# Kernel optimization log

Hardware: AMD Instinct MI355X
Metric: run time of the kernel (lower is better)

The kernel has to match this reference:

```python
import jax, jax.numpy as jnp
import numpy as np

VOCAB = 50000
DIM = 300
BATCH = 1024
CTX = 10


def setup_inputs() -> dict:
    key = jax.random.key(0)
    k1, k2, k3, k4 = jax.random.split(key, 4)
    context = jax.random.randint(k1, (BATCH, CTX), 0, VOCAB, dtype=jnp.int64 if jax.config.read('jax_enable_x64') else jnp.int32)
    W_proj = jax.random.normal(k2, (DIM, VOCAB), dtype=jnp.float32) * 0.02
    W_cls = jax.random.normal(k3, (VOCAB, DIM), dtype=jnp.float32) * 0.02
    b_cls = jax.random.normal(k4, (VOCAB,), dtype=jnp.float32) * 0.02
    return {"context": context, "W_proj": W_proj, "W_cls": W_cls, "b_cls": b_cls, "pad_idx": 0}


def reference(context, W_proj, W_cls, b_cls, pad_idx):
    # One-hot @ W_proj.T == gather of W_proj columns at context ids: [B, C, D]
    emb = jnp.take(W_proj, context, axis=1)            # [D, B, C]
    emb = jnp.moveaxis(emb, 0, -1)                     # [B, C, D]
    # zeroing the pad_idx column of the one-hot kills pad tokens' contribution,
    # but the mean still divides by the full context length C.
    mask = (context != pad_idx).astype(emb.dtype)      # [B, C]
    emb = emb * mask[..., None]
    pooled = emb.mean(axis=1)                          # [B, D]
    logits = pooled @ W_cls.T + b_cls                  # [B, V]
    return jax.nn.log_softmax(logits, axis=1)
```

## Files before the change

kernel.cpp:

```cpp
#include <hip/hip_runtime.h>
#include <math.h>

#define B_SZ 1024
#define CTXL 10
#define DIM  300
#define VOC  50000
#define KP   320
#define NTIL 391
#define NSG  50
#define WROW 1200
#define WMAXOFF 59999984

typedef short s16x8 __attribute__((ext_vector_type(8)));
typedef float f32x4 __attribute__((ext_vector_type(4)));

__global__ void transpose_kernel(const float* __restrict__ W, float* __restrict__ WT) {
  __shared__ float tile[32][33];
  const int v0 = blockIdx.x * 32, d0 = blockIdx.y * 32;
  const int tx = threadIdx.x & 31, ty = threadIdx.x >> 5;
#pragma unroll
  for (int i = 0; i < 32; i += 8) {
    const int d = d0 + ty + i, v = v0 + tx;
    tile[ty + i][tx] = (d < DIM && v < VOC) ? W[d * VOC + v] : 0.f;
  }
  __syncthreads();
#pragma unroll
  for (int i = 0; i < 32; i += 8) {
    const int v = v0 + ty + i, d = d0 + tx;
    if (v < VOC && d < DIM) WT[v * DIM + d] = tile[tx][ty + i];
  }
}

__global__ void pool_kernel(const int* __restrict__ ctx, const float* __restrict__ WT,
                            const int* __restrict__ padp, __bf16* __restrict__ pooled) {
  const int b = blockIdx.x;
  const int d = threadIdx.x;
  const int pad = *padp;
  float s = 0.f;
  if (d < DIM) {
#pragma unroll
    for (int c = 0; c < CTXL; ++c) {
      const int id = ctx[b * CTXL + c];
      if (id != pad) s += WT[id * DIM + d];
    }
  }
  pooled[b * KP + d] = (__bf16)(s * 0.1f);
}

__global__ __launch_bounds__(256, 2) void gemm_kernel(const __bf16* __restrict__ A,
                                                      const float* __restrict__ Wcls,
                                                      const float* __restrict__ bias,
                                                      float* __restrict__ out) {
  const int bid = blockIdx.x;
  const int s = bid & 7;
  const int mj = (bid >> 3) & 7;
  const int G = bid >> 6;
  const int nt = G * 8 + s;
  if (nt >= NTIL) return;
  const int m0 = mj * 128;
  const int n0 = nt * 128;
  const int t = threadIdx.x;
  const int lane = t & 63;
  const int wave = t >> 6;
  const int wm = wave >> 1, wn = wave & 1;
  const int fr = lane & 15;
  const int hi = lane >> 4;

  f32x4 acc[4][4];
#pragma unroll
  for (int i = 0; i < 4; ++i)
#pragma unroll
    for (int j = 0; j < 4; ++j) acc[i][j] = (f32x4){0.f, 0.f, 0.f, 0.f};

  const char* Ab = (const char*)A;
  const char* Wb = (const char*)Wcls;

  int aoff[4];
#pragma unroll
  for (int mf = 0; mf < 4; ++mf)
    aoff[mf] = (m0 + wm * 64 + mf * 16 + fr) * (KP * 2);
  int boff[4];
#pragma unroll
  for (int nf = 0; nf < 4; ++nf) {
    int r = n0 + wn * 64 + nf * 16 + fr;
    if (r > VOC - 1) r = VOC - 1;
    boff[nf] = r * WROW;
  }

#pragma unroll
  for (int ks = 0; ks < 10; ++ks) {
    const int koff = ks * 32 + hi * 8;
    s16x8 af[4];
#pragma unroll
    for (int mf = 0; mf < 4; ++mf)
      af[mf] = *(const s16x8*)(Ab + aoff[mf] + koff * 2);
    s16x8 bf[4];
#pragma unroll
    for (int nf = 0; nf < 4; ++nf) {
      int o0 = boff[nf] + koff * 4;
      int o1 = o0 + 16;
      if (o0 > WMAXOFF) o0 = WMAXOFF;
      if (o1 > WMAXOFF) o1 = WMAXOFF;
      const f32x4 x0 = *(const f32x4*)(Wb + o0);
      const f32x4 x1 = *(const f32x4*)(Wb + o1);
      union { __bf16 h; short v; } cv;
      s16x8 bb;
      cv.h = (__bf16)x0[0]; bb[0] = cv.v;
      cv.h = (__bf16)x0[1]; bb[1] = cv.v;
      cv.h = (__bf16)x0[2]; bb[2] = cv.v;
      cv.h = (__bf16)x0[3]; bb[3] = cv.v;
      cv.h = (__bf16)x1[0]; bb[4] = cv.v;
      cv.h = (__bf16)x1[1]; bb[5] = cv.v;
      cv.h = (__bf16)x1[2]; bb[6] = cv.v;
      cv.h = (__bf16)x1[3]; bb[7] = cv.v;
      bf[nf] = bb;
    }
#pragma unroll
    for (int mf = 0; mf < 4; ++mf)
#pragma unroll
      for (int nf = 0; nf < 4; ++nf)
        acc[mf][nf] = __builtin_amdgcn_mfma_f32_16x16x32_bf16(af[mf], bf[nf], acc[mf][nf], 0, 0, 0);
  }

#pragma unroll
  for (int nf = 0; nf < 4; ++nf) {
    const int col = n0 + wn * 64 + nf * 16 + fr;
    if (col < VOC) {
      const float bia = bias[col];
#pragma unroll
      for (int mf = 0; mf < 4; ++mf)
#pragma unroll
        for (int reg = 0; reg < 4; ++reg) {
          const int row = m0 + wm * 64 + mf * 16 + hi * 4 + reg;
          out[row * VOC + col] = acc[mf][nf][reg] + bia;
        }
    }
  }
}

__global__ __launch_bounds__(1024) void softfix_kernel(float* __restrict__ out) {
  __shared__ float red[16];
  const int b = blockIdx.x;
  const int tid = threadIdx.x;
  float4* rowp = (float4*)(out + b * VOC);

  float s = 0.f;
  for (int i = tid; i < VOC / 4; i += 1024) {
    const float4 v = rowp[i];
    s += __expf(v.x) + __expf(v.y) + __expf(v.z) + __expf(v.w);
  }
#pragma unroll
  for (int off = 1; off < 64; off <<= 1) s += __shfl_xor(s, off, 64);
  if ((tid & 63) == 0) red[tid >> 6] = s;
  __syncthreads();
  float tot = 0.f;
#pragma unroll
  for (int j = 0; j < 16; ++j) tot += red[j];
  const float l = logf(tot);

  for (int i = tid; i < VOC / 4; i += 1024) {
    float4 v = rowp[i];
    v.x -= l; v.y -= l; v.z -= l; v.w -= l;
    rowp[i] = v;
  }
}

extern "C" void kernel_launch(void* const* d_in, const int* in_sizes, int n_in,
                              void* d_out, int out_size, void* d_ws, size_t ws_size,
                              hipStream_t stream) {
  (void)in_sizes; (void)out_size;
  if (n_in < 5) return;
  const int*   ctx   = (const int*)d_in[0];
  const float* Wproj = (const float*)d_in[1];
  const float* Wcls  = (const float*)d_in[2];
  const float* bcls  = (const float*)d_in[3];
  const int*   padp  = (const int*)d_in[4];
  float* out = (float*)d_out;

  if (ws_size < 655360) return;
  __bf16* pooled = (__bf16*)d_ws;
  float*  WT     = out;

  transpose_kernel<<<dim3(1563, 10), 256, 0, stream>>>(Wproj, WT);
  pool_kernel<<<B_SZ, KP, 0, stream>>>(ctx, WT, padp, pooled);
  gemm_kernel<<<NSG * 64, 256, 0, stream>>>(pooled, Wcls, bcls, out);
  softfix_kernel<<<B_SZ, 1024, 0, stream>>>(out);
}
```

Before: 547.8 us.

## Pre-pack classifier weights and pooled activations into bf16 MFMA-ready tiles

Adds a kernel that converts W_cls to bf16 and stores it in contiguous 8KB per-tile, per-k-step blocks. The pooling kernel also writes pooled activations in the same blocked layout. The GEMM then does plain vector loads with no inline fp32-to-bf16 conversion or clamping, which aims to cut redundant fp32 reads across M-tiles and improve load coalescing. In exchange it adds an extra pass over W_cls and needs about 32MB more workspace; launch bounds are also raised to 3 waves per SIMD.

```diff
diff --git a/kernel.cpp b/kernel.cpp
--- a/kernel.cpp
+++ b/kernel.cpp
@@ -5,13 +5,15 @@
 #define CTXL 10
 #define DIM  300
 #define VOC  50000
-#define KP   320
 #define NTIL 391
 #define NSG  50
 #define WROW 1200
-#define WMAXOFF 59999984
+#define BPACK_BYTES 32030720
+#define APACK_BYTES 655360
+#define WS_NEED     (BPACK_BYTES + APACK_BYTES)
 
 typedef short s16x8 __attribute__((ext_vector_type(8)));
+typedef short s16x4 __attribute__((ext_vector_type(4)));
 typedef float f32x4 __attribute__((ext_vector_type(4)));
 
 __global__ void transpose_kernel(const float* __restrict__ W, float* __restrict__ WT) {
@@ -32,7 +34,7 @@
 }
 
 __global__ void pool_kernel(const int* __restrict__ ctx, const float* __restrict__ WT,
-                            const int* __restrict__ padp, __bf16* __restrict__ pooled) {
+                            const int* __restrict__ padp, char* __restrict__ apack) {
   const int b = blockIdx.x;
   const int d = threadIdx.x;
   const int pad = *padp;
@@ -44,11 +46,34 @@
       if (id != pad) s += WT[id * DIM + d];
     }
   }
-  pooled[b * KP + d] = (__bf16)(s * 0.1f);
+  union { __bf16 h; short v; } cv;
+  cv.h = (__bf16)(s * 0.1f);
+  *(short*)(apack + ((b >> 7) * 10 + (d >> 5)) * 8192 + (b & 127) * 64 + (d & 31) * 2) = cv.v;
 }
 
-__global__ __launch_bounds__(256, 2) void gemm_kernel(const __bf16* __restrict__ A,
-                                                      const float* __restrict__ Wcls,
+__global__ void bpack_kernel(const float* __restrict__ Wcls, char* __restrict__ bpack) {
+  const int nt = blockIdx.x;
+  const int cl = (int)(threadIdx.x >> 3);
+  const int o  = (int)(threadIdx.x & 7);
+  const int colg = blockIdx.y * 32 + cl;
+  const int v = nt * 128 + colg;
+#pragma unroll
+  for (int ks = 0; ks < 10; ++ks) {
+    f32x4 x = (f32x4){0.f, 0.f, 0.f, 0.f};
+    if (v < VOC && (ks < 9 || o < 3))
+      x = *(const f32x4*)((const char*)Wcls + v * WROW + ks * 128 + o * 16);
+    union { __bf16 h; short s; } cv;
+    s16x4 b4;
+    cv.h = (__bf16)x[0]; b4[0] = cv.s;
+    cv.h = (__bf16)x[1]; b4[1] = cv.s;
+    cv.h = (__bf16)x[2]; b4[2] = cv.s;
+    cv.h = (__bf16)x[3]; b4[3] = cv.s;
+    *(s16x4*)(bpack + (nt * 10 + ks) * 8192 + colg * 64 + o * 8) = b4;
+  }
+}
+
+__global__ __launch_bounds__(256, 3) void gemm_kernel(const char* __restrict__ apack,
+                                                      const char* __restrict__ bpack,
                                                       const float* __restrict__ bias,
                                                       float* __restrict__ out) {
   const int bid = blockIdx.x;
@@ -59,9 +84,8 @@
   if (nt >= NTIL) return;
   const int m0 = mj * 128;
   const int n0 = nt * 128;
-  const int t = threadIdx.x;
-  const int lane = t & 63;
-  const int wave = t >> 6;
+  const int lane = (int)(threadIdx.x & 63);
+  const int wave = (int)(threadIdx.x >> 6);
   const int wm = wave >> 1, wn = wave & 1;
   const int fr = lane & 15;
   const int hi = lane >> 4;
@@ -72,49 +96,24 @@
 #pragma unroll
     for (int j = 0; j < 4; ++j) acc[i][j] = (f32x4){0.f, 0.f, 0.f, 0.f};
 
-  const char* Ab = (const char*)A;
-  const char* Wb = (const char*)Wcls;
-
-  int aoff[4];
+  int aoff[4], boff[4];
 #pragma unroll
-  for (int mf = 0; mf < 4; ++mf)
-    aoff[mf] = (m0 + wm * 64 + mf * 16 + fr) * (KP * 2);
-  int boff[4];
-#pragma unroll
-  for (int nf = 0; nf < 4; ++nf) {
-    int r = n0 + wn * 64 + nf * 16 + fr;
-    if (r > VOC - 1) r = VOC - 1;
-    boff[nf] = r * WROW;
+  for (int f = 0; f < 4; ++f) {
+    aoff[f] = (wm * 64 + f * 16 + fr) * 64 + hi * 16;
+    boff[f] = (wn * 64 + f * 16 + fr) * 64 + hi * 16;
   }
+  const char* Ab = apack + mj * (10 * 8192);
+  const char* Bb = bpack + nt * (10 * 8192);
 
 #pragma unroll
   for (int ks = 0; ks < 10; ++ks) {
-    const int koff = ks * 32 + hi * 8;
-    s16x8 af[4];
+    const char* Ablk = Ab + ks * 8192;
+    const char* Bblk = Bb + ks * 8192;
+    s16x8 af[4], bf[4];
 #pragma unroll
-    for (int mf = 0; mf < 4; ++mf)
-      af[mf] = *(const s16x8*)(Ab + aoff[mf] + koff * 2);
-    s16x8 bf[4];
+    for (int mf = 0; mf < 4; ++mf) af[mf] = *(const s16x8*)(Ablk + aoff[mf]);
 #pragma unroll
-    for (int nf = 0; nf < 4; ++nf) {
-      int o0 = boff[nf] + koff * 4;
-      int o1 = o0 + 16;
-      if (o0 > WMAXOFF) o0 = WMAXOFF;
-      if (o1 > WMAXOFF) o1 = WMAXOFF;
-      const f32x4 x0 = *(const f32x4*)(Wb + o0);
-      const f32x4 x1 = *(const f32x4*)(Wb + o1);
-      union { __bf16 h; short v; } cv;
-      s16x8 bb;
-      cv.h = (__bf16)x0[0]; bb[0] = cv.v;
-      cv.h = (__bf16)x0[1]; bb[1] = cv.v;
-      cv.h = (__bf16)x0[2]; bb[2] = cv.v;
-      cv.h = (__bf16)x0[3]; bb[3] = cv.v;
-      cv.h = (__bf16)x1[0]; bb[4] = cv.v;
-      cv.h = (__bf16)x1[1]; bb[5] = cv.v;
-      cv.h = (__bf16)x1[2]; bb[6] = cv.v;
-      cv.h = (__bf16)x1[3]; bb[7] = cv.v;
-      bf[nf] = bb;
-    }
+    for (int nf = 0; nf < 4; ++nf) bf[nf] = *(const s16x8*)(Bblk + boff[nf]);
 #pragma unroll
     for (int mf = 0; mf < 4; ++mf)
 #pragma unroll
@@ -177,12 +176,14 @@
   const int*   padp  = (const int*)d_in[4];
   float* out = (float*)d_out;
 
-  if (ws_size < 655360) return;
-  __bf16* pooled = (__bf16*)d_ws;
-  float*  WT     = out;
+  if (ws_size < WS_NEED) return;
+  char* bpack = (char*)d_ws;
+  char* apack = (char*)d_ws + BPACK_BYTES;
+  float* WT   = out;
 
+  bpack_kernel<<<dim3(NTIL, 4), 256, 0, stream>>>(Wcls, bpack);
   transpose_kernel<<<dim3(1563, 10), 256, 0, stream>>>(Wproj, WT);
-  pool_kernel<<<B_SZ, KP, 0, stream>>>(ctx, WT, padp, pooled);
-  gemm_kernel<<<NSG * 64, 256, 0, stream>>>(pooled, Wcls, bcls, out);
+  pool_kernel<<<B_SZ, 320, 0, stream>>>(ctx, WT, padp, apack);
+  gemm_kernel<<<NSG * 64, 256, 0, stream>>>(apack, bpack, bcls, out);
   softfix_kernel<<<B_SZ, 1024, 0, stream>>>(out);
 }
```

New measurement: 502.0 us. 1.09x faster.
